# Performance work log

Measured on AMD Instinct MI355X. Metric: run time of the kernel, lower is better.

Reference implementation:

```python
import jax, jax.numpy as jnp
import numpy as np

H = 128

def _gru_layer(x_seq, Wih, Whh, bih, bhh):
    # x_seq: [B, T, I] -> hidden sequence [B, T, H]
    B, T, _ = x_seq.shape
    # precompute all input projections for the whole sequence (gate order: r, z, n)
    xi = jnp.einsum('bti,gi->btg', x_seq, Wih) + bih  # [B, T, 3H]
    def step(h, xt):
        gh = h @ Whh.T + bhh                           # [B, 3H]
        xr, xz, xn = xt[:, :H], xt[:, H:2*H], xt[:, 2*H:]
        hr, hz, hn = gh[:, :H], gh[:, H:2*H], gh[:, 2*H:]
        r = jax.nn.sigmoid(xr + hr)
        z = jax.nn.sigmoid(xz + hz)
        n = jnp.tanh(xn + r * hn)
        h_new = (1.0 - z) * n + z * h
        return h_new, h_new
    h0 = jnp.zeros((B, H), dtype=x_seq.dtype)
    _, hs = jax.lax.scan(step, h0, jnp.swapaxes(xi, 0, 1))  # hs: [T, B, H]
    return jnp.swapaxes(hs, 0, 1)


def setup_inputs() -> dict:
    key = jax.random.key(0)
    ks = jax.random.split(key, 12)
    s = 1.0 / np.sqrt(H)
    inp = {
        'x': jax.random.normal(ks[0], (512, 512, 5), dtype=jnp.float32),
        'Wih0': jax.random.uniform(ks[1], (3*H, 5), minval=-s, maxval=s, dtype=jnp.float32),
        'Whh0': jax.random.uniform(ks[2], (3*H, H), minval=-s, maxval=s, dtype=jnp.float32),
        'bih0': jax.random.uniform(ks[3], (3*H,), minval=-s, maxval=s, dtype=jnp.float32),
        'bhh0': jax.random.uniform(ks[4], (3*H,), minval=-s, maxval=s, dtype=jnp.float32),
        'Wih_rest': jax.random.uniform(ks[5], (3, 3*H, H), minval=-s, maxval=s, dtype=jnp.float32),
        'Whh_rest': jax.random.uniform(ks[6], (3, 3*H, H), minval=-s, maxval=s, dtype=jnp.float32),
        'bih_rest': jax.random.uniform(ks[7], (3, 3*H), minval=-s, maxval=s, dtype=jnp.float32),
        'bhh_rest': jax.random.uniform(ks[8], (3, 3*H), minval=-s, maxval=s, dtype=jnp.float32),
        'fc_w': jax.random.uniform(ks[9], (1, H), minval=-s, maxval=s, dtype=jnp.float32),
        'fc_b': jax.random.uniform(ks[10], (1,), minval=-s, maxval=s, dtype=jnp.float32),
    }
    return inp


def reference(x, Wih0, Whh0, bih0, bhh0, Wih_rest, Whh_rest, bih_rest, bhh_rest, fc_w, fc_b):
    # 4-layer GRU, batch_first, h0 = zeros; dropout in eval mode = identity.
    out = _gru_layer(x, Wih0, Whh0, bih0, bhh0)
    for l in range(3):
        out = _gru_layer(out, Wih_rest[l], Whh_rest[l], bih_rest[l], bhh_rest[l])
    last = out[:, -1, :]                     # [B, H]
    return last @ fc_w.T + fc_b              # [B, 1]
```

## Files before the change

### kernel.cpp

```cpp
#include <hip/hip_runtime.h>
#include <cmath>

#define HH   128
#define G3   384
#define TT   512
#define BTOT 512
#define BB   2
#define WT   32
#define NBLK (BTOT / BB)
#define NTHR 512

__device__ __forceinline__ float sigmoidf_(float x) {
    return 1.0f / (1.0f + __expf(-x));
}
__device__ __forceinline__ float tanhf_(float x) {
    float e = __expf(2.0f * x);
    return 1.0f - 2.0f / (e + 1.0f);
}
__device__ __forceinline__ void lds_barrier() {
    asm volatile("s_waitcnt lgkmcnt(0)" ::: "memory");
    __builtin_amdgcn_s_barrier();
}

template <bool FIRST, bool LAST>
__global__ __launch_bounds__(NTHR, 2) void gru_layer(
    const float* in, float* out,
    const float* __restrict__ Wih, const float* __restrict__ Whh,
    const float* __restrict__ bih, const float* __restrict__ bhh,
    const float* __restrict__ fcw, const float* __restrict__ fcb,
    float* __restrict__ fcout) {
    const int tid = threadIdx.x;
    const int kt  = tid & 3;
    const int gt  = tid >> 2;
    const int b0  = blockIdx.x * BB;

    __shared__ __align__(16) float s_h[2][BB][4][36];
    __shared__ __align__(16) float s_in[FIRST ? (BB * TT * 5) : (BB * WT * HH)];
    __shared__ __align__(16) float s_xi[FIRST ? 4 : (BB * WT * G3)];

    float wh[3][32];
#pragma unroll
    for (int i = 0; i < 3; ++i) {
        const float* wr = Whh + (size_t)(i * HH + gt) * HH + kt * 32;
#pragma unroll
        for (int j = 0; j < 32; j += 4) {
            float4 v = *(const float4*)(wr + j);
            wh[i][j] = v.x; wh[i][j + 1] = v.y; wh[i][j + 2] = v.z; wh[i][j + 3] = v.w;
        }
    }
#pragma unroll
    for (int i = 0; i < 3; ++i)
#pragma unroll
        for (int j = 0; j < 32; ++j) asm volatile("" : "+v"(wh[i][j]));

    float wx5[3][5];
    if constexpr (FIRST) {
#pragma unroll
        for (int i = 0; i < 3; ++i)
#pragma unroll
            for (int j = 0; j < 5; ++j) wx5[i][j] = Wih[(i * HH + gt) * 5 + j];
    }

    const float br  = bih[gt] + bhh[gt];
    const float bz  = bih[HH + gt] + bhh[HH + gt];
    const float bxn = bih[2 * HH + gt];
    const float bhn = bhh[2 * HH + gt];

    if (tid < BB * HH) {
        int bb = tid >> 7, j = tid & (HH - 1);
        s_h[0][bb][j >> 5][j & 31] = 0.0f;
    }
    if constexpr (FIRST) {
#pragma unroll
        for (int r = 0; r < (BB * TT * 5) / NTHR; ++r) {
            int idx = r * NTHR + tid;
            s_in[idx] = in[(size_t)b0 * TT * 5 + idx];
        }
    }
    __syncthreads();

    for (int w = 0; w < TT / WT; ++w) {
        if constexpr (!FIRST) {
#pragma unroll
            for (int i = 0; i < 3; ++i)
#pragma unroll
                for (int j = 0; j < 32; ++j) asm volatile("" : "+v"(wh[i][j]));

            {
                const size_t gbase = (size_t)b0 * TT * HH + (size_t)w * WT * HH;
#pragma unroll
                for (int r = 0; r < 4; ++r) {
                    int idx = r * NTHR + tid;
                    int bb  = idx >> 10;
                    int rem = idx & 1023;
                    float4 v = *(const float4*)&in[gbase + (size_t)bb * TT * HH +
                                                   (size_t)(rem >> 5) * HH + (rem & 31) * 4];
                    *(float4*)&s_in[idx * 4] = v;
                }
            }
            lds_barrier();

            {
                const int g  = tid & 127;
                const int tq = tid >> 7;
                const float* w0p = Wih + (size_t)g * HH;
                const float* w1p = Wih + (size_t)(HH + g) * HH;
                const float* w2p = Wih + (size_t)(2 * HH + g) * HH;
                float acc[BB][3][8];
#pragma unroll
                for (int bb = 0; bb < BB; ++bb)
#pragma unroll
                    for (int i = 0; i < 3; ++i)
#pragma unroll
                        for (int tt = 0; tt < 8; ++tt) acc[bb][i][tt] = 0.0f;
#pragma unroll 2
                for (int kc = 0; kc < 32; ++kc) {
                    float4 wa = *(const float4*)(w0p + kc * 4);
                    float4 wb = *(const float4*)(w1p + kc * 4);
                    float4 wc = *(const float4*)(w2p + kc * 4);
#pragma unroll
                    for (int bb = 0; bb < BB; ++bb)
#pragma unroll
                        for (int tt = 0; tt < 8; ++tt) {
                            float4 sv = *(const float4*)&s_in[bb * (WT * HH) +
                                                              (tq * 8 + tt) * HH + kc * 4];
                            acc[bb][0][tt] = fmaf(wa.x, sv.x, acc[bb][0][tt]);
                            acc[bb][0][tt] = fmaf(wa.y, sv.y, acc[bb][0][tt]);
                            acc[bb][0][tt] = fmaf(wa.z, sv.z, acc[bb][0][tt]);
                            acc[bb][0][tt] = fmaf(wa.w, sv.w, acc[bb][0][tt]);
                            acc[bb][1][tt] = fmaf(wb.x, sv.x, acc[bb][1][tt]);
                            acc[bb][1][tt] = fmaf(wb.y, sv.y, acc[bb][1][tt]);
                            acc[bb][1][tt] = fmaf(wb.z, sv.z, acc[bb][1][tt]);
                            acc[bb][1][tt] = fmaf(wb.w, sv.w, acc[bb][1][tt]);
                            acc[bb][2][tt] = fmaf(wc.x, sv.x, acc[bb][2][tt]);
                            acc[bb][2][tt] = fmaf(wc.y, sv.y, acc[bb][2][tt]);
                            acc[bb][2][tt] = fmaf(wc.z, sv.z, acc[bb][2][tt]);
                            acc[bb][2][tt] = fmaf(wc.w, sv.w, acc[bb][2][tt]);
                        }
                }
#pragma unroll
                for (int bb = 0; bb < BB; ++bb)
#pragma unroll
                    for (int tt = 0; tt < 8; ++tt) {
                        int tok = tq * 8 + tt;
                        s_xi[bb * (WT * G3) + tok * G3 + g]          = acc[bb][0][tt];
                        s_xi[bb * (WT * G3) + tok * G3 + HH + g]     = acc[bb][1][tt];
                        s_xi[bb * (WT * G3) + tok * G3 + 2 * HH + g] = acc[bb][2][tt];
                    }
            }
            lds_barrier();
        }

        for (int tw = 0; tw < WT; ++tw) {
            const int t   = w * WT + tw;
            const int cur = t & 1;

            float a00 = 0.f, a01 = 0.f, a02 = 0.f, a10 = 0.f, a11 = 0.f, a12 = 0.f;
            const float* hp0 = &s_h[cur][0][kt][0];
            const float* hp1 = &s_h[cur][1][kt][0];
#pragma unroll
            for (int jj = 0; jj < 32; jj += 4) {
                float4 u = *(const float4*)(hp0 + jj);
                float4 v = *(const float4*)(hp1 + jj);
                a00 = fmaf(wh[0][jj], u.x, a00); a00 = fmaf(wh[0][jj+1], u.y, a00);
                a00 = fmaf(wh[0][jj+2], u.z, a00); a00 = fmaf(wh[0][jj+3], u.w, a00);
                a01 = fmaf(wh[1][jj], u.x, a01); a01 = fmaf(wh[1][jj+1], u.y, a01);
                a01 = fmaf(wh[1][jj+2], u.z, a01); a01 = fmaf(wh[1][jj+3], u.w, a01);
                a02 = fmaf(wh[2][jj], u.x, a02); a02 = fmaf(wh[2][jj+1], u.y, a02);
                a02 = fmaf(wh[2][jj+2], u.z, a02); a02 = fmaf(wh[2][jj+3], u.w, a02);
                a10 = fmaf(wh[0][jj], v.x, a10); a10 = fmaf(wh[0][jj+1], v.y, a10);
                a10 = fmaf(wh[0][jj+2], v.z, a10); a10 = fmaf(wh[0][jj+3], v.w, a10);
                a11 = fmaf(wh[1][jj], v.x, a11); a11 = fmaf(wh[1][jj+1], v.y, a11);
                a11 = fmaf(wh[1][jj+2], v.z, a11); a11 = fmaf(wh[1][jj+3], v.w, a11);
                a12 = fmaf(wh[2][jj], v.x, a12); a12 = fmaf(wh[2][jj+1], v.y, a12);
                a12 = fmaf(wh[2][jj+2], v.z, a12); a12 = fmaf(wh[2][jj+3], v.w, a12);
            }
            a00 += __shfl_xor(a00, 1, 64); a00 += __shfl_xor(a00, 2, 64);
            a01 += __shfl_xor(a01, 1, 64); a01 += __shfl_xor(a01, 2, 64);
            a02 += __shfl_xor(a02, 1, 64); a02 += __shfl_xor(a02, 2, 64);
            a10 += __shfl_xor(a10, 1, 64); a10 += __shfl_xor(a10, 2, 64);
            a11 += __shfl_xor(a11, 1, 64); a11 += __shfl_xor(a11, 2, 64);
            a12 += __shfl_xor(a12, 1, 64); a12 += __shfl_xor(a12, 2, 64);

            if (kt < 2) {
                const int bb = kt;
                float cr  = (kt == 0) ? a00 : a10;
                float cz  = (kt == 0) ? a01 : a11;
                float cnh = (kt == 0) ? a02 : a12;
                float xr, xz, xn;
                if constexpr (FIRST) {
                    const float* xp = &s_in[bb * (TT * 5) + t * 5];
                    float x0 = xp[0], x1 = xp[1], x2 = xp[2], x3 = xp[3], x4 = xp[4];
                    xr = wx5[0][0]*x0 + wx5[0][1]*x1 + wx5[0][2]*x2 + wx5[0][3]*x3 + wx5[0][4]*x4;
                    xz = wx5[1][0]*x0 + wx5[1][1]*x1 + wx5[1][2]*x2 + wx5[1][3]*x3 + wx5[1][4]*x4;
                    xn = wx5[2][0]*x0 + wx5[2][1]*x1 + wx5[2][2]*x2 + wx5[2][3]*x3 + wx5[2][4]*x4;
                } else {
                    const float* xp = &s_xi[bb * (WT * G3) + tw * G3];
                    xr = xp[gt]; xz = xp[HH + gt]; xn = xp[2 * HH + gt];
                }
                float r = sigmoidf_(xr + cr + br);
                float z = sigmoidf_(xz + cz + bz);
                float n = tanhf_(xn + bxn + r * (cnh + bhn));
                float hp = s_h[cur][bb][gt >> 5][gt & 31];
                float hv = (1.0f - z) * n + z * hp;
                s_h[cur ^ 1][bb][gt >> 5][gt & 31] = hv;
                if constexpr (!LAST)
                    out[((size_t)(b0 + bb) * TT + t) * HH + gt] = hv;
            }
            lds_barrier();
        }
    }

    if constexpr (LAST) {
        if (tid < 128) {
            int bb = tid >> 6, l = tid & 63;
            float h0 = s_h[0][bb][l >> 5][l & 31];
            float h1 = s_h[0][bb][(l >> 5) + 2][l & 31];
            float s = h0 * fcw[l] + h1 * fcw[l + 64];
#pragma unroll
            for (int m = 32; m >= 1; m >>= 1) s += __shfl_xor(s, m, 64);
            if (l == 0) fcout[b0 + bb] = s + fcb[0];
        }
    }
}

extern "C" void kernel_launch(void* const* d_in, const int* in_sizes, int n_in,
                              void* d_out, int out_size, void* d_ws, size_t ws_size,
                              hipStream_t stream) {
    const float* x    = (const float*)d_in[0];
    const float* Wih0 = (const float*)d_in[1];
    const float* Whh0 = (const float*)d_in[2];
    const float* bih0 = (const float*)d_in[3];
    const float* bhh0 = (const float*)d_in[4];
    const float* WihR = (const float*)d_in[5];
    const float* WhhR = (const float*)d_in[6];
    const float* bihR = (const float*)d_in[7];
    const float* bhhR = (const float*)d_in[8];
    const float* fcw  = (const float*)d_in[9];
    const float* fcb  = (const float*)d_in[10];

    float* buf = (float*)d_ws;

    gru_layer<true, false><<<NBLK, NTHR, 0, stream>>>(x, buf, Wih0, Whh0, bih0, bhh0,
                                                      nullptr, nullptr, nullptr);
    gru_layer<false, false><<<NBLK, NTHR, 0, stream>>>(buf, buf, WihR, WhhR, bihR, bhhR,
                                                       nullptr, nullptr, nullptr);
    gru_layer<false, false><<<NBLK, NTHR, 0, stream>>>(buf, buf, WihR + G3 * HH,
                                                       WhhR + G3 * HH, bihR + G3, bhhR + G3,
                                                       nullptr, nullptr, nullptr);
    gru_layer<false, true><<<NBLK, NTHR, 0, stream>>>(buf, buf, WihR + 2 * G3 * HH,
                                                      WhhR + 2 * G3 * HH, bihR + 2 * G3,
                                                      bhhR + 2 * G3, fcw, fcb, (float*)d_out);
}
```

Measured before the change: 3.438 ms.

## Process one batch element per block to double grid size and occupancy

```diff
diff --git a/kernel.cpp b/kernel.cpp
--- a/kernel.cpp
+++ b/kernel.cpp
@@ -5,9 +5,8 @@
 #define G3   384
 #define TT   512
 #define BTOT 512
-#define BB   2
-#define WT   32
-#define NBLK (BTOT / BB)
+#define WT   16
+#define NBLK BTOT
 #define NTHR 512
 
 __device__ __forceinline__ float sigmoidf_(float x) {
@@ -23,7 +22,7 @@
 }
 
 template <bool FIRST, bool LAST>
-__global__ __launch_bounds__(NTHR, 2) void gru_layer(
+__global__ __launch_bounds__(NTHR, 4) void gru_layer(
     const float* in, float* out,
     const float* __restrict__ Wih, const float* __restrict__ Whh,
     const float* __restrict__ bih, const float* __restrict__ bhh,
@@ -32,11 +31,11 @@
     const int tid = threadIdx.x;
     const int kt  = tid & 3;
     const int gt  = tid >> 2;
-    const int b0  = blockIdx.x * BB;
-
-    __shared__ __align__(16) float s_h[2][BB][4][36];
-    __shared__ __align__(16) float s_in[FIRST ? (BB * TT * 5) : (BB * WT * HH)];
-    __shared__ __align__(16) float s_xi[FIRST ? 4 : (BB * WT * G3)];
+    const int b   = blockIdx.x;
+
+    __shared__ __align__(16) float s_h[2][4][36];
+    __shared__ __align__(16) float s_in[FIRST ? (TT * 5) : (WT * HH)];
+    __shared__ __align__(16) float s_xi[FIRST ? 4 : (WT * G3)];
 
     float wh[3][32];
 #pragma unroll
@@ -66,37 +65,22 @@
     const float bxn = bih[2 * HH + gt];
     const float bhn = bhh[2 * HH + gt];
 
-    if (tid < BB * HH) {
-        int bb = tid >> 7, j = tid & (HH - 1);
-        s_h[0][bb][j >> 5][j & 31] = 0.0f;
-    }
+    if (tid < HH) s_h[0][tid >> 5][tid & 31] = 0.0f;
     if constexpr (FIRST) {
 #pragma unroll
-        for (int r = 0; r < (BB * TT * 5) / NTHR; ++r) {
+        for (int r = 0; r < 5; ++r) {
             int idx = r * NTHR + tid;
-            s_in[idx] = in[(size_t)b0 * TT * 5 + idx];
+            s_in[idx] = in[(size_t)b * TT * 5 + idx];
         }
     }
     __syncthreads();
 
     for (int w = 0; w < TT / WT; ++w) {
         if constexpr (!FIRST) {
-#pragma unroll
-            for (int i = 0; i < 3; ++i)
-#pragma unroll
-                for (int j = 0; j < 32; ++j) asm volatile("" : "+v"(wh[i][j]));
-
             {
-                const size_t gbase = (size_t)b0 * TT * HH + (size_t)w * WT * HH;
-#pragma unroll
-                for (int r = 0; r < 4; ++r) {
-                    int idx = r * NTHR + tid;
-                    int bb  = idx >> 10;
-                    int rem = idx & 1023;
-                    float4 v = *(const float4*)&in[gbase + (size_t)bb * TT * HH +
-                                                   (size_t)(rem >> 5) * HH + (rem & 31) * 4];
-                    *(float4*)&s_in[idx * 4] = v;
-                }
+                int tok = tid >> 5, k4 = (tid & 31) * 4;
+                float4 v = *(const float4*)&in[((size_t)b * TT + w * WT + tok) * HH + k4];
+                *(float4*)&s_in[tok * HH + k4] = v;
             }
             lds_barrier();
 
@@ -106,47 +90,40 @@
                 const float* w0p = Wih + (size_t)g * HH;
                 const float* w1p = Wih + (size_t)(HH + g) * HH;
                 const float* w2p = Wih + (size_t)(2 * HH + g) * HH;
-                float acc[BB][3][8];
-#pragma unroll
-                for (int bb = 0; bb < BB; ++bb)
-#pragma unroll
-                    for (int i = 0; i < 3; ++i)
-#pragma unroll
-                        for (int tt = 0; tt < 8; ++tt) acc[bb][i][tt] = 0.0f;
-#pragma unroll 2
+                float acc[3][4];
+#pragma unroll
+                for (int i = 0; i < 3; ++i)
+#pragma unroll
+                    for (int tt = 0; tt < 4; ++tt) acc[i][tt] = 0.0f;
+#pragma unroll 4
                 for (int kc = 0; kc < 32; ++kc) {
                     float4 wa = *(const float4*)(w0p + kc * 4);
                     float4 wb = *(const float4*)(w1p + kc * 4);
                     float4 wc = *(const float4*)(w2p + kc * 4);
 #pragma unroll
-                    for (int bb = 0; bb < BB; ++bb)
-#pragma unroll
-                        for (int tt = 0; tt < 8; ++tt) {
-                            float4 sv = *(const float4*)&s_in[bb * (WT * HH) +
-                                                              (tq * 8 + tt) * HH + kc * 4];
-                            acc[bb][0][tt] = fmaf(wa.x, sv.x, acc[bb][0][tt]);
-                            acc[bb][0][tt] = fmaf(wa.y, sv.y, acc[bb][0][tt]);
-                            acc[bb][0][tt] = fmaf(wa.z, sv.z, acc[bb][0][tt]);
-                            acc[bb][0][tt] = fmaf(wa.w, sv.w, acc[bb][0][tt]);
-                            acc[bb][1][tt] = fmaf(wb.x, sv.x, acc[bb][1][tt]);
-                            acc[bb][1][tt] = fmaf(wb.y, sv.y, acc[bb][1][tt]);
-                            acc[bb][1][tt] = fmaf(wb.z, sv.z, acc[bb][1][tt]);
-                            acc[bb][1][tt] = fmaf(wb.w, sv.w, acc[bb][1][tt]);
-                            acc[bb][2][tt] = fmaf(wc.x, sv.x, acc[bb][2][tt]);
-                            acc[bb][2][tt] = fmaf(wc.y, sv.y, acc[bb][2][tt]);
-                            acc[bb][2][tt] = fmaf(wc.z, sv.z, acc[bb][2][tt]);
-                            acc[bb][2][tt] = fmaf(wc.w, sv.w, acc[bb][2][tt]);
-                        }
+                    for (int tt = 0; tt < 4; ++tt) {
+                        float4 sv = *(const float4*)&s_in[(tq * 4 + tt) * HH + kc * 4];
+                        acc[0][tt] = fmaf(wa.x, sv.x, acc[0][tt]);
+                        acc[0][tt] = fmaf(wa.y, sv.y, acc[0][tt]);
+                        acc[0][tt] = fmaf(wa.z, sv.z, acc[0][tt]);
+                        acc[0][tt] = fmaf(wa.w, sv.w, acc[0][tt]);
+                        acc[1][tt] = fmaf(wb.x, sv.x, acc[1][tt]);
+                        acc[1][tt] = fmaf(wb.y, sv.y, acc[1][tt]);
+                        acc[1][tt] = fmaf(wb.z, sv.z, acc[1][tt]);
+                        acc[1][tt] = fmaf(wb.w, sv.w, acc[1][tt]);
+                        acc[2][tt] = fmaf(wc.x, sv.x, acc[2][tt]);
+                        acc[2][tt] = fmaf(wc.y, sv.y, acc[2][tt]);
+                        acc[2][tt] = fmaf(wc.z, sv.z, acc[2][tt]);
+                        acc[2][tt] = fmaf(wc.w, sv.w, acc[2][tt]);
+                    }
                 }
 #pragma unroll
-                for (int bb = 0; bb < BB; ++bb)
-#pragma unroll
-                    for (int tt = 0; tt < 8; ++tt) {
-                        int tok = tq * 8 + tt;
-                        s_xi[bb * (WT * G3) + tok * G3 + g]          = acc[bb][0][tt];
-                        s_xi[bb * (WT * G3) + tok * G3 + HH + g]     = acc[bb][1][tt];
-                        s_xi[bb * (WT * G3) + tok * G3 + 2 * HH + g] = acc[bb][2][tt];
-                    }
+                for (int tt = 0; tt < 4; ++tt) {
+                    int tok = tq * 4 + tt;
+                    s_xi[tok * G3 + g]          = acc[0][tt];
+                    s_xi[tok * G3 + HH + g]     = acc[1][tt];
+                    s_xi[tok * G3 + 2 * HH + g] = acc[2][tt];
+                }
             }
             lds_barrier();
         }
@@ -155,71 +132,55 @@
             const int t   = w * WT + tw;
             const int cur = t & 1;
 
-            float a00 = 0.f, a01 = 0.f, a02 = 0.f, a10 = 0.f, a11 = 0.f, a12 = 0.f;
-            const float* hp0 = &s_h[cur][0][kt][0];
-            const float* hp1 = &s_h[cur][1][kt][0];
+            float a0 = 0.f, a1 = 0.f, a2 = 0.f;
+            const float* hp = &s_h[cur][kt][0];
 #pragma unroll
             for (int jj = 0; jj < 32; jj += 4) {
-                float4 u = *(const float4*)(hp0 + jj);
-                float4 v = *(const float4*)(hp1 + jj);
-                a00 = fmaf(wh[0][jj], u.x, a00); a00 = fmaf(wh[0][jj+1], u.y, a00);
-                a00 = fmaf(wh[0][jj+2], u.z, a00); a00 = fmaf(wh[0][jj+3], u.w, a00);
-                a01 = fmaf(wh[1][jj], u.x, a01); a01 = fmaf(wh[1][jj+1], u.y, a01);
-                a01 = fmaf(wh[1][jj+2], u.z, a01); a01 = fmaf(wh[1][jj+3], u.w, a01);
-                a02 = fmaf(wh[2][jj], u.x, a02); a02 = fmaf(wh[2][jj+1], u.y, a02);
-                a02 = fmaf(wh[2][jj+2], u.z, a02); a02 = fmaf(wh[2][jj+3], u.w, a02);
-                a10 = fmaf(wh[0][jj], v.x, a10); a10 = fmaf(wh[0][jj+1], v.y, a10);
-                a10 = fmaf(wh[0][jj+2], v.z, a10); a10 = fmaf(wh[0][jj+3], v.w, a10);
-                a11 = fmaf(wh[1][jj], v.x, a11); a11 = fmaf(wh[1][jj+1], v.y, a11);
-                a11 = fmaf(wh[1][jj+2], v.z, a11); a11 = fmaf(wh[1][jj+3], v.w, a11);
-                a12 = fmaf(wh[2][jj], v.x, a12); a12 = fmaf(wh[2][jj+1], v.y, a12);
-                a12 = fmaf(wh[2][jj+2], v.z, a12); a12 = fmaf(wh[2][jj+3], v.w, a12);
-            }
-            a00 += __shfl_xor(a00, 1, 64); a00 += __shfl_xor(a00, 2, 64);
-            a01 += __shfl_xor(a01, 1, 64); a01 += __shfl_xor(a01, 2, 64);
-            a02 += __shfl_xor(a02, 1, 64); a02 += __shfl_xor(a02, 2, 64);
-            a10 += __shfl_xor(a10, 1, 64); a10 += __shfl_xor(a10, 2, 64);
-            a11 += __shfl_xor(a11, 1, 64); a11 += __shfl_xor(a11, 2, 64);
-            a12 += __shfl_xor(a12, 1, 64); a12 += __shfl_xor(a12, 2, 64);
-
-            if (kt < 2) {
-                const int bb = kt;
-                float cr  = (kt == 0) ? a00 : a10;
-                float cz  = (kt == 0) ? a01 : a11;
-                float cnh = (kt == 0) ? a02 : a12;
+                float4 u = *(const float4*)(hp + jj);
+                a0 = fmaf(wh[0][jj], u.x, a0); a0 = fmaf(wh[0][jj+1], u.y, a0);
+                a0 = fmaf(wh[0][jj+2], u.z, a0); a0 = fmaf(wh[0][jj+3], u.w, a0);
+                a1 = fmaf(wh[1][jj], u.x, a1); a1 = fmaf(wh[1][jj+1], u.y, a1);
+                a1 = fmaf(wh[1][jj+2], u.z, a1); a1 = fmaf(wh[1][jj+3], u.w, a1);
+                a2 = fmaf(wh[2][jj], u.x, a2); a2 = fmaf(wh[2][jj+1], u.y, a2);
+                a2 = fmaf(wh[2][jj+2], u.z, a2); a2 = fmaf(wh[2][jj+3], u.w, a2);
+            }
+            a0 += __shfl_xor(a0, 1, 64); a0 += __shfl_xor(a0, 2, 64);
+            a1 += __shfl_xor(a1, 1, 64); a1 += __shfl_xor(a1, 2, 64);
+            a2 += __shfl_xor(a2, 1, 64); a2 += __shfl_xor(a2, 2, 64);
+
+            if (kt == 0) {
                 float xr, xz, xn;
                 if constexpr (FIRST) {
-                    const float* xp = &s_in[bb * (TT * 5) + t * 5];
+                    const float* xp = &s_in[t * 5];
                     float x0 = xp[0], x1 = xp[1], x2 = xp[2], x3 = xp[3], x4 = xp[4];
                     xr = wx5[0][0]*x0 + wx5[0][1]*x1 + wx5[0][2]*x2 + wx5[0][3]*x3 + wx5[0][4]*x4;
                     xz = wx5[1][0]*x0 + wx5[1][1]*x1 + wx5[1][2]*x2 + wx5[1][3]*x3 + wx5[1][4]*x4;
                     xn = wx5[2][0]*x0 + wx5[2][1]*x1 + wx5[2][2]*x2 + wx5[2][3]*x3 + wx5[2][4]*x4;
                 } else {
-                    const float* xp = &s_xi[bb * (WT * G3) + tw * G3];
+                    const float* xp = &s_xi[tw * G3];
                     xr = xp[gt]; xz = xp[HH + gt]; xn = xp[2 * HH + gt];
                 }
-                float r = sigmoidf_(xr + cr + br);
-                float z = sigmoidf_(xz + cz + bz);
-                float n = tanhf_(xn + bxn + r * (cnh + bhn));
-                float hp = s_h[cur][bb][gt >> 5][gt & 31];
-                float hv = (1.0f - z) * n + z * hp;
-                s_h[cur ^ 1][bb][gt >> 5][gt & 31] = hv;
+                float r = sigmoidf_(xr + a0 + br);
+                float z = sigmoidf_(xz + a1 + bz);
+                float n = tanhf_(xn + bxn + r * (a2 + bhn));
+                float hp_ = s_h[cur][gt >> 5][gt & 31];
+                float hv  = (1.0f - z) * n + z * hp_;
+                s_h[cur ^ 1][gt >> 5][gt & 31] = hv;
                 if constexpr (!LAST)
-                    out[((size_t)(b0 + bb) * TT + t) * HH + gt] = hv;
+                    out[((size_t)b * TT + t) * HH + gt] = hv;
             }
             lds_barrier();
         }
     }
 
     if constexpr (LAST) {
-        if (tid < 128) {
-            int bb = tid >> 6, l = tid & 63;
-            float h0 = s_h[0][bb][l >> 5][l & 31];
-            float h1 = s_h[0][bb][(l >> 5) + 2][l & 31];
-            float s = h0 * fcw[l] + h1 * fcw[l + 64];
+        if (tid < 64) {
+            float h0 = s_h[0][tid >> 5][tid & 31];
+            float h1 = s_h[0][(tid >> 5) + 2][tid & 31];
+            float s = h0 * fcw[tid] + h1 * fcw[tid + 64];
 #pragma unroll
             for (int m = 32; m >= 1; m >>= 1) s += __shfl_xor(s, m, 64);
-            if (l == 0) fcout[b0 + bb] = s + fcb[0];
+            if (tid == 0) fcout[b] = s + fcb[0];
         }
     }
 }
```

After: 7.036 ms. +104.7%, slower.
